# Optimization experiments

Hardware: AMD Instinct MI355X
Metric: run time of the kernel (lower is better)

The kernel has to match this reference:

```python
import jax, jax.numpy as jnp
import numpy as np

N = 8192      # num nodes == embedding vocab
E = 524288    # num edges (avg degree 64)
IN, HID, OUT = 128, 256, 128


def setup_inputs() -> dict:
    key = jax.random.key(0)
    ks = jax.random.split(key, 7)
    x = jax.random.randint(ks[0], (N,), 0, N)
    edge_index = jax.random.randint(ks[1], (2, E), 0, N)
    emb_table = jax.random.normal(ks[2], (N, IN), jnp.float32) * 0.02
    W1 = jax.random.normal(ks[3], (IN, HID), jnp.float32) * (1.0 / np.sqrt(IN))
    b1 = jnp.zeros((HID,), jnp.float32)
    W2 = jax.random.normal(ks[4], (HID, OUT), jnp.float32) * (1.0 / np.sqrt(HID))
    b2 = jnp.zeros((OUT,), jnp.float32)
    return {"x": x, "edge_index": edge_index, "emb_table": emb_table,
            "W1": W1, "b1": b1, "W2": W2, "b2": b2}


def gcn_conv(h, edge_index, W, b):
    # PyG GCNConv with add_self_loops=True, symmetric normalization.
    n = h.shape[0]
    src, dst = edge_index[0], edge_index[1]
    h = h @ W                                            # [N, F_out]
    # degree of each target node, including the implicit self-loop (+1)
    deg = jax.ops.segment_sum(jnp.ones((src.shape[0],), h.dtype), dst,
                              num_segments=n) + 1.0
    dinv = jax.lax.rsqrt(deg)                            # deg >= 1 always
    norm = dinv[src] * dinv[dst]                         # [E]
    agg = jax.ops.segment_sum(h[src] * norm[:, None], dst, num_segments=n)
    agg = agg + h * (dinv * dinv)[:, None]               # self-loop message
    return agg + b


def reference(x, edge_index, emb_table, W1, b1, W2, b2):
    h = emb_table[x]                                     # embedding lookup [N, IN]
    h = jax.nn.relu(gcn_conv(h, edge_index, W1, b1))
    z = gcn_conv(h, edge_index, W2, b2)                  # [N, OUT]
    return jax.nn.sigmoid(z @ z.T)                       # dense decode [N, N]
```

## Files before the change

kernel.cpp:

```cpp
#include <hip/hip_runtime.h>
#include <hip/hip_bf16.h>

#define NN 8192
#define NE 524288

typedef __attribute__((ext_vector_type(4))) float f32x4;
typedef __attribute__((ext_vector_type(8))) short s16x8;


__global__ void zero_i32(int* __restrict__ p, int n) {
    int i = blockIdx.x * blockDim.x + threadIdx.x;
    if (i < n) p[i] = 0;
}

__global__ void count_edges(const int* __restrict__ dst, int* __restrict__ cnt) {
    int e = blockIdx.x * blockDim.x + threadIdx.x;
    if (e < NE) atomicAdd(&cnt[dst[e]], 1);
}

__global__ __launch_bounds__(256) void scan_deg(const int* __restrict__ cnt,
                                                int* __restrict__ rowoff,
                                                int* __restrict__ cursor,
                                                float* __restrict__ dinv) {
    __shared__ int part[256];
    int t = threadIdx.x;
    int local[32];
    int s = 0;
#pragma unroll
    for (int i = 0; i < 32; i++) { local[i] = cnt[t * 32 + i]; s += local[i]; }
    part[t] = s;
    __syncthreads();
    for (int off = 1; off < 256; off <<= 1) {
        int v = (t >= off) ? part[t - off] : 0;
        __syncthreads();
        part[t] += v;
        __syncthreads();
    }
    int run = (t == 0) ? 0 : part[t - 1];
#pragma unroll
    for (int i = 0; i < 32; i++) {
        int n = t * 32 + i;
        rowoff[n] = run;
        cursor[n] = run;
        dinv[n] = rsqrtf((float)local[i] + 1.0f);
        run += local[i];
    }
    if (t == 255) rowoff[NN] = run;
}

__global__ void fill_csr(const int* __restrict__ src, const int* __restrict__ dst,
                         int* __restrict__ cursor, int* __restrict__ csr_src) {
    int e = blockIdx.x * blockDim.x + threadIdx.x;
    if (e < NE) {
        int d = dst[e];
        int pos = atomicAdd(&cursor[d], 1);
        csr_src[pos] = src[e];
    }
}


__global__ void prep_w(const float* __restrict__ W1, const float* __restrict__ W2,
                       __hip_bfloat16* __restrict__ W1t, __hip_bfloat16* __restrict__ W2t) {
    int i = blockIdx.x * blockDim.x + threadIdx.x;
    if (i < 128 * 256) {
        int n = i >> 7, k = i & 127;
        W1t[i] = __float2bfloat16(W1[k * 256 + n]);
    } else {
        int j = i - 128 * 256;
        int n = j >> 8, k = j & 255;
        W2t[j] = __float2bfloat16(W2[k * 128 + n]);
    }
}


__global__ __launch_bounds__(256) void agg_embed(
    const int* __restrict__ x, const float* __restrict__ emb,
    const int* __restrict__ csr_src, const int* __restrict__ rowoff,
    const float* __restrict__ dinv, __hip_bfloat16* __restrict__ htb)
{
    int wave = threadIdx.x >> 6;
    int lane = threadIdx.x & 63;
    int node = (blockIdx.x << 2) + wave;
    int e0 = rowoff[node], e1 = rowoff[node + 1];
    const float2* emb2 = reinterpret_cast<const float2*>(emb);
    float ax = 0.f, ay = 0.f;
#pragma unroll 4
    for (int e = e0; e < e1; ++e) {
        int s = csr_src[e];
        float ds = dinv[s];
        float2 v = emb2[(size_t)x[s] * 64 + lane];
        ax = fmaf(ds, v.x, ax);
        ay = fmaf(ds, v.y, ay);
    }
    float dn = dinv[node];
    float2 hv = emb2[(size_t)x[node] * 64 + lane];
    float rx = fmaf(dn, ax, dn * dn * hv.x);
    float ry = fmaf(dn, ay, dn * dn * hv.y);
    htb[node * 128 + lane * 2]     = __float2bfloat16(rx);
    htb[node * 128 + lane * 2 + 1] = __float2bfloat16(ry);
}


__global__ __launch_bounds__(256) void agg_final(
    const float* __restrict__ g,
    const int* __restrict__ csr_src, const int* __restrict__ rowoff,
    const float* __restrict__ dinv, const float* __restrict__ b2,
    __hip_bfloat16* __restrict__ zb)
{
    int wave = threadIdx.x >> 6;
    int lane = threadIdx.x & 63;
    int node = (blockIdx.x << 2) + wave;
    int e0 = rowoff[node], e1 = rowoff[node + 1];
    const float2* g2 = reinterpret_cast<const float2*>(g);
    float ax = 0.f, ay = 0.f;
#pragma unroll 4
    for (int e = e0; e < e1; ++e) {
        int s = csr_src[e];
        float ds = dinv[s];
        float2 v = g2[s * 64 + lane];
        ax = fmaf(ds, v.x, ax);
        ay = fmaf(ds, v.y, ay);
    }
    float dn = dinv[node];
    float2 hv = g2[node * 64 + lane];
    float2 bb = reinterpret_cast<const float2*>(b2)[lane];
    float rx = fmaf(dn, ax, dn * dn * hv.x) + bb.x;
    float ry = fmaf(dn, ay, dn * dn * hv.y) + bb.y;
    zb[node * 128 + lane * 2]     = __float2bfloat16(rx);
    zb[node * 128 + lane * 2 + 1] = __float2bfloat16(ry);
}


__global__ __launch_bounds__(256) void gemm1_mfma(
    const ushort* __restrict__ htb, const ushort* __restrict__ W1t,
    const float* __restrict__ b1, __hip_bfloat16* __restrict__ h1b)
{
    int lane = threadIdx.x & 63;
    int wn = threadIdx.x >> 6;
    int row0 = blockIdx.x * 64;
    int col0 = wn * 64;
    int fr = lane & 15;
    int kq = lane >> 4;

    f32x4 acc[4][4];
#pragma unroll
    for (int i = 0; i < 4; i++)
#pragma unroll
        for (int j = 0; j < 4; j++) acc[i][j] = (f32x4){0.f, 0.f, 0.f, 0.f};

#pragma unroll
    for (int k0 = 0; k0 < 128; k0 += 32) {
        s16x8 a[4], b[4];
#pragma unroll
        for (int i = 0; i < 4; i++) {
            a[i] = *reinterpret_cast<const s16x8*>(htb + (row0 + i * 16 + fr) * 128 + k0 + kq * 8);
            b[i] = *reinterpret_cast<const s16x8*>(W1t + (col0 + i * 16 + fr) * 128 + k0 + kq * 8);
        }
#pragma unroll
        for (int i = 0; i < 4; i++)
#pragma unroll
            for (int j = 0; j < 4; j++)
                acc[i][j] = __builtin_amdgcn_mfma_f32_16x16x32_bf16(a[i], b[j], acc[i][j], 0, 0, 0);
    }

#pragma unroll
    for (int j = 0; j < 4; j++) {
        float bv = b1[col0 + j * 16 + fr];
#pragma unroll
        for (int i = 0; i < 4; i++)
#pragma unroll
            for (int r = 0; r < 4; r++) {
                int row = row0 + i * 16 + kq * 4 + r;
                int col = col0 + j * 16 + fr;
                float v = acc[i][j][r] + bv;
                v = v > 0.f ? v : 0.f;
                h1b[row * 256 + col] = __float2bfloat16(v);
            }
    }
}


__global__ __launch_bounds__(256) void gemm2_mfma(
    const ushort* __restrict__ h1b, const ushort* __restrict__ W2t,
    float* __restrict__ g)
{
    int lane = threadIdx.x & 63;
    int wn = threadIdx.x >> 6;
    int row0 = blockIdx.x * 64;
    int col0 = wn * 32;
    int fr = lane & 15;
    int kq = lane >> 4;

    f32x4 acc[4][2];
#pragma unroll
    for (int i = 0; i < 4; i++)
#pragma unroll
        for (int j = 0; j < 2; j++) acc[i][j] = (f32x4){0.f, 0.f, 0.f, 0.f};

#pragma unroll
    for (int k0 = 0; k0 < 256; k0 += 32) {
        s16x8 a[4], b[2];
#pragma unroll
        for (int i = 0; i < 4; i++)
            a[i] = *reinterpret_cast<const s16x8*>(h1b + (row0 + i * 16 + fr) * 256 + k0 + kq * 8);
#pragma unroll
        for (int j = 0; j < 2; j++)
            b[j] = *reinterpret_cast<const s16x8*>(W2t + (col0 + j * 16 + fr) * 256 + k0 + kq * 8);
#pragma unroll
        for (int i = 0; i < 4; i++)
#pragma unroll
            for (int j = 0; j < 2; j++)
                acc[i][j] = __builtin_amdgcn_mfma_f32_16x16x32_bf16(a[i], b[j], acc[i][j], 0, 0, 0);
    }

#pragma unroll
    for (int i = 0; i < 4; i++)
#pragma unroll
        for (int j = 0; j < 2; j++)
#pragma unroll
            for (int r = 0; r < 4; r++) {
                int row = row0 + i * 16 + kq * 4 + r;
                int col = col0 + j * 16 + fr;
                g[row * 128 + col] = acc[i][j][r];
            }
}


__global__ __launch_bounds__(256) void decode(const ushort* __restrict__ zb,
                                              float* __restrict__ out) {
    int lane = threadIdx.x & 63;
    int wave = threadIdx.x >> 6;
    int wm = wave >> 1, wn = wave & 1;
    int row0 = blockIdx.y * 128 + wm * 64;
    int col0 = blockIdx.x * 128 + wn * 64;
    int fr = lane & 15;
    int kq = lane >> 4;

    f32x4 acc[4][4];
#pragma unroll
    for (int i = 0; i < 4; i++)
#pragma unroll
        for (int j = 0; j < 4; j++) acc[i][j] = (f32x4){0.f, 0.f, 0.f, 0.f};

#pragma unroll
    for (int k0 = 0; k0 < 128; k0 += 32) {
        s16x8 a[4], b[4];
#pragma unroll
        for (int i = 0; i < 4; i++) {
            a[i] = *reinterpret_cast<const s16x8*>(zb + (size_t)(row0 + i * 16 + fr) * 128 + k0 + kq * 8);
            b[i] = *reinterpret_cast<const s16x8*>(zb + (size_t)(col0 + i * 16 + fr) * 128 + k0 + kq * 8);
        }
#pragma unroll
        for (int i = 0; i < 4; i++)
#pragma unroll
            for (int j = 0; j < 4; j++)
                acc[i][j] = __builtin_amdgcn_mfma_f32_16x16x32_bf16(a[i], b[j], acc[i][j], 0, 0, 0);
    }

#pragma unroll
    for (int i = 0; i < 4; i++)
#pragma unroll
        for (int j = 0; j < 4; j++)
#pragma unroll
            for (int r = 0; r < 4; r++) {
                int row = row0 + i * 16 + kq * 4 + r;
                int col = col0 + j * 16 + fr;
                float v = acc[i][j][r];
                out[(size_t)row * NN + col] = 1.0f / (1.0f + __expf(-v));
            }
}


extern "C" void kernel_launch(void* const* d_in, const int* in_sizes, int n_in,
                              void* d_out, int out_size, void* d_ws, size_t ws_size,
                              hipStream_t stream) {
    const int*   x    = (const int*)d_in[0];
    const int*   esrc = (const int*)d_in[1];
    const int*   edst = (const int*)d_in[1] + NE;
    const float* emb  = (const float*)d_in[2];
    const float* W1   = (const float*)d_in[3];
    const float* b1   = (const float*)d_in[4];
    const float* W2   = (const float*)d_in[5];
    const float* b2   = (const float*)d_in[6];
    float* out = (float*)d_out;

    char* ws = (char*)d_ws;
    size_t off = 0;
    auto alloc = [&](size_t bytes) -> void* {
        void* p = ws + off;
        off = (off + bytes + 255) & ~(size_t)255;
        return p;
    };
    int*   cnt    = (int*)alloc(NN * 4);
    int*   rowoff = (int*)alloc((NN + 1) * 4);
    int*   cursor = (int*)alloc(NN * 4);
    float* dinv   = (float*)alloc(NN * 4);
    int*   csr    = (int*)alloc(NE * 4);
    __hip_bfloat16* W1t = (__hip_bfloat16*)alloc(128 * 256 * 2);
    __hip_bfloat16* W2t = (__hip_bfloat16*)alloc(256 * 128 * 2);
    __hip_bfloat16* htb = (__hip_bfloat16*)alloc((size_t)NN * 128 * 2);
    __hip_bfloat16* h1b = (__hip_bfloat16*)alloc((size_t)NN * 256 * 2);
    float*          gbuf= (float*)alloc((size_t)NN * 128 * 4);
    __hip_bfloat16* zb  = (__hip_bfloat16*)alloc((size_t)NN * 128 * 2);

    zero_i32<<<NN / 256, 256, 0, stream>>>(cnt, NN);
    count_edges<<<NE / 256, 256, 0, stream>>>(edst, cnt);
    scan_deg<<<1, 256, 0, stream>>>(cnt, rowoff, cursor, dinv);
    fill_csr<<<NE / 256, 256, 0, stream>>>(esrc, edst, cursor, csr);

    prep_w<<<(2 * 128 * 256) / 256, 256, 0, stream>>>(W1, W2, W1t, W2t);

    agg_embed<<<NN / 4, 256, 0, stream>>>(x, emb, csr, rowoff, dinv, htb);
    gemm1_mfma<<<NN / 64, 256, 0, stream>>>((const ushort*)htb, (const ushort*)W1t, b1, h1b);

    gemm2_mfma<<<NN / 64, 256, 0, stream>>>((const ushort*)h1b, (const ushort*)W2t, gbuf);
    agg_final<<<NN / 4, 256, 0, stream>>>(gbuf, csr, rowoff, dinv, b2, zb);

    decode<<<dim3(64, 64), 256, 0, stream>>>((const ushort*)zb, out);
}
```

Before: 460.0 us.

## Pre-scale features by source dinv and gather in bf16 during aggregation

Features are pre-multiplied by each source node's dinv and stored in bf16, in a new embed_s kernel for layer 1 and in the gemm2 epilogue for layer 2. The aggregation kernels then only sum gathered bf16 values, with no per-edge dinv or x indirection, and the self-loop is folded in as an extra term. This halves the bytes per gathered row and removes dependent loads on the edge loop. It costs one extra small kernel and pass, and adds bf16 rounding before accumulation; the sigmoid in decode also switches to exp2/rcp intrinsics.

```diff
diff --git a/kernel.cpp b/kernel.cpp
--- a/kernel.cpp
+++ b/kernel.cpp
@@ -6,6 +6,10 @@
 
 typedef __attribute__((ext_vector_type(4))) float f32x4;
 typedef __attribute__((ext_vector_type(8))) short s16x8;
+
+__device__ __forceinline__ float bf2f(ushort u) {
+    return __uint_as_float((unsigned)u << 16);
+}
 
 
 __global__ void zero_i32(int* __restrict__ p, int n) {
@@ -73,61 +77,46 @@
 }
 
 
-__global__ __launch_bounds__(256) void agg_embed(
-    const int* __restrict__ x, const float* __restrict__ emb,
-    const int* __restrict__ csr_src, const int* __restrict__ rowoff,
-    const float* __restrict__ dinv, __hip_bfloat16* __restrict__ htb)
+__global__ void embed_s(const int* __restrict__ x, const float* __restrict__ emb,
+                        const float* __restrict__ dinv, __hip_bfloat16* __restrict__ hbs) {
+    int i = blockIdx.x * blockDim.x + threadIdx.x;
+    int n = i >> 7, c = i & 127;
+    hbs[i] = __float2bfloat16(dinv[n] * emb[(size_t)x[n] * 128 + c]);
+}
+
+
+template <bool ADD_BIAS>
+__global__ __launch_bounds__(256) void aggregate_bf16(
+    const ushort* __restrict__ S, const int* __restrict__ csr_src,
+    const int* __restrict__ rowoff, const float* __restrict__ dinv,
+    const float* __restrict__ bias, __hip_bfloat16* __restrict__ out)
 {
     int wave = threadIdx.x >> 6;
     int lane = threadIdx.x & 63;
     int node = (blockIdx.x << 2) + wave;
     int e0 = rowoff[node], e1 = rowoff[node + 1];
-    const float2* emb2 = reinterpret_cast<const float2*>(emb);
+    const uint* S2 = reinterpret_cast<const uint*>(S);
     float ax = 0.f, ay = 0.f;
-#pragma unroll 4
+#pragma unroll 8
     for (int e = e0; e < e1; ++e) {
         int s = csr_src[e];
-        float ds = dinv[s];
-        float2 v = emb2[(size_t)x[s] * 64 + lane];
-        ax = fmaf(ds, v.x, ax);
-        ay = fmaf(ds, v.y, ay);
+        uint v = S2[s * 64 + lane];
+        ax += bf2f((ushort)(v & 0xffff));
+        ay += bf2f((ushort)(v >> 16));
+    }
+    {
+        uint v = S2[node * 64 + lane];
+        ax += bf2f((ushort)(v & 0xffff));
+        ay += bf2f((ushort)(v >> 16));
     }
     float dn = dinv[node];
-    float2 hv = emb2[(size_t)x[node] * 64 + lane];
-    float rx = fmaf(dn, ax, dn * dn * hv.x);
-    float ry = fmaf(dn, ay, dn * dn * hv.y);
-    htb[node * 128 + lane * 2]     = __float2bfloat16(rx);
-    htb[node * 128 + lane * 2 + 1] = __float2bfloat16(ry);
-}
-
-
-__global__ __launch_bounds__(256) void agg_final(
-    const float* __restrict__ g,
-    const int* __restrict__ csr_src, const int* __restrict__ rowoff,
-    const float* __restrict__ dinv, const float* __restrict__ b2,
-    __hip_bfloat16* __restrict__ zb)
-{
-    int wave = threadIdx.x >> 6;
-    int lane = threadIdx.x & 63;
-    int node = (blockIdx.x << 2) + wave;
-    int e0 = rowoff[node], e1 = rowoff[node + 1];
-    const float2* g2 = reinterpret_cast<const float2*>(g);
-    float ax = 0.f, ay = 0.f;
-#pragma unroll 4
-    for (int e = e0; e < e1; ++e) {
-        int s = csr_src[e];
-        float ds = dinv[s];
-        float2 v = g2[s * 64 + lane];
-        ax = fmaf(ds, v.x, ax);
-        ay = fmaf(ds, v.y, ay);
-    }
-    float dn = dinv[node];
-    float2 hv = g2[node * 64 + lane];
-    float2 bb = reinterpret_cast<const float2*>(b2)[lane];
-    float rx = fmaf(dn, ax, dn * dn * hv.x) + bb.x;
-    float ry = fmaf(dn, ay, dn * dn * hv.y) + bb.y;
-    zb[node * 128 + lane * 2]     = __float2bfloat16(rx);
-    zb[node * 128 + lane * 2 + 1] = __float2bfloat16(ry);
+    float rx = dn * ax, ry = dn * ay;
+    if (ADD_BIAS) {
+        float2 bb = reinterpret_cast<const float2*>(bias)[lane];
+        rx += bb.x; ry += bb.y;
+    }
+    out[node * 128 + lane * 2]     = __float2bfloat16(rx);
+    out[node * 128 + lane * 2 + 1] = __float2bfloat16(ry);
 }
 
 
@@ -182,7 +171,7 @@
 
 __global__ __launch_bounds__(256) void gemm2_mfma(
     const ushort* __restrict__ h1b, const ushort* __restrict__ W2t,
-    float* __restrict__ g)
+    const float* __restrict__ dinv, __hip_bfloat16* __restrict__ gb2)
 {
     int lane = threadIdx.x & 63;
     int wn = threadIdx.x >> 6;
@@ -216,13 +205,15 @@
 #pragma unroll
     for (int i = 0; i < 4; i++)
 #pragma unroll
-        for (int j = 0; j < 2; j++)
-#pragma unroll
-            for (int r = 0; r < 4; r++) {
-                int row = row0 + i * 16 + kq * 4 + r;
+        for (int r = 0; r < 4; r++) {
+            int row = row0 + i * 16 + kq * 4 + r;
+            float dv = dinv[row];
+#pragma unroll
+            for (int j = 0; j < 2; j++) {
                 int col = col0 + j * 16 + fr;
-                g[row * 128 + col] = acc[i][j][r];
+                gb2[row * 128 + col] = __float2bfloat16(dv * acc[i][j][r]);
             }
+        }
 }
 
 
@@ -266,7 +257,8 @@
                 int row = row0 + i * 16 + kq * 4 + r;
                 int col = col0 + j * 16 + fr;
                 float v = acc[i][j][r];
-                out[(size_t)row * NN + col] = 1.0f / (1.0f + __expf(-v));
+                float ev = __builtin_amdgcn_exp2f(v * -1.442695041f);
+                out[(size_t)row * NN + col] = __builtin_amdgcn_rcpf(1.0f + ev);
             }
 }
 
@@ -298,9 +290,10 @@
     int*   csr    = (int*)alloc(NE * 4);
     __hip_bfloat16* W1t = (__hip_bfloat16*)alloc(128 * 256 * 2);
     __hip_bfloat16* W2t = (__hip_bfloat16*)alloc(256 * 128 * 2);
+    __hip_bfloat16* hbs = (__hip_bfloat16*)alloc((size_t)NN * 128 * 2);
     __hip_bfloat16* htb = (__hip_bfloat16*)alloc((size_t)NN * 128 * 2);
     __hip_bfloat16* h1b = (__hip_bfloat16*)alloc((size_t)NN * 256 * 2);
-    float*          gbuf= (float*)alloc((size_t)NN * 128 * 4);
+    __hip_bfloat16* gb2 = (__hip_bfloat16*)alloc((size_t)NN * 128 * 2);
     __hip_bfloat16* zb  = (__hip_bfloat16*)alloc((size_t)NN * 128 * 2);
 
     zero_i32<<<NN / 256, 256, 0, stream>>>(cnt, NN);
@@ -310,11 +303,13 @@
 
     prep_w<<<(2 * 128 * 256) / 256, 256, 0, stream>>>(W1, W2, W1t, W2t);
 
-    agg_embed<<<NN / 4, 256, 0, stream>>>(x, emb, csr, rowoff, dinv, htb);
+    embed_s<<<NN * 128 / 256, 256, 0, stream>>>(x, emb, dinv, hbs);
+
+    aggregate_bf16<false><<<NN / 4, 256, 0, stream>>>((const ushort*)hbs, csr, rowoff, dinv, nullptr, htb);
     gemm1_mfma<<<NN / 64, 256, 0, stream>>>((const ushort*)htb, (const ushort*)W1t, b1, h1b);
 
-    gemm2_mfma<<<NN / 64, 256, 0, stream>>>((const ushort*)h1b, (const ushort*)W2t, gbuf);
-    agg_final<<<NN / 4, 256, 0, stream>>>(gbuf, csr, rowoff, dinv, b2, zb);
+    gemm2_mfma<<<NN / 64, 256, 0, stream>>>((const ushort*)h1b, (const ushort*)W2t, dinv, gb2);
+    aggregate_bf16<true><<<NN / 4, 256, 0, stream>>>((const ushort*)gb2, csr, rowoff, dinv, b2, zb);
 
     decode<<<dim3(64, 64), 256, 0, stream>>>((const ushort*)zb, out);
 }
```

Measured after the change: 428.6 us. -6.8%, faster.
